# Performance work log

Hardware: AMD Instinct MI355X
Metric: run time of the kernel (lower is better)

Reference implementation:

```python
import jax, jax.numpy as jnp
import numpy as np

N_NODES = 50000
N_EDGES = 600000
DIM = 128


def setup_inputs() -> dict:
    key = jax.random.key(0)
    k1, k2, k3, k4, k5, k6 = jax.random.split(key, 6)
    return {
        "h_v": jax.random.normal(k1, (N_NODES, DIM), dtype=jnp.float32),
        "h_d": jax.random.normal(k2, (N_EDGES, DIM), dtype=jnp.float32),
        "W_pi": jax.random.normal(k3, (DIM, 1), dtype=jnp.float32) * (1.0 / np.sqrt(DIM)),
        "W_M": jax.random.normal(k4, (2 * DIM, 1), dtype=jnp.float32) * (1.0 / np.sqrt(2 * DIM)),
        "src": jax.random.randint(k5, (N_EDGES,), 0, N_NODES, dtype=jnp.int64) if jax.config.jax_enable_x64 else jax.random.randint(k5, (N_EDGES,), 0, N_NODES, dtype=jnp.int32),
        "dst": jax.random.randint(k6, (N_EDGES,), 0, N_NODES, dtype=jnp.int32),
    }


def reference(h_v, h_d, W_pi, W_M, src, dst):
    # Gather per-edge endpoint features: [E, dim]
    ft_s = h_v[src]
    ft_d = h_v[dst]
    prod = ft_s * ft_d                                   # u_mul_v
    # e = pi(src*dst*d): [E, 1]
    e = (prod * h_d) @ W_pi
    # mask = sigmoid(M(cat([src*dst, d]))): [E, 1]
    mask = jax.nn.sigmoid(jnp.concatenate([prod, h_d], axis=-1) @ W_M)
    logits = (e * mask)[:, 0]                            # [E]
    # edge_softmax grouped by destination node (DGL semantics)
    seg_max = jax.ops.segment_max(logits, dst, num_segments=N_NODES)
    ex = jnp.exp(logits - seg_max[dst])
    seg_sum = jax.ops.segment_sum(ex, dst, num_segments=N_NODES)
    a = ex / seg_sum[dst]                                # [E]
    # dropout_local is identity at inference
    # message m = ft_src * a; aggregate sum over incoming edges per dst node
    out = jax.ops.segment_sum(ft_s * a[:, None], dst, num_segments=N_NODES)
    return out
```

## Files before the change

### kernel.cpp

```cpp
#include <hip/hip_runtime.h>

#define NN 50000
#define NE 600000
#define DIM 128
#define NB 196


__global__ __launch_bounds__(256) void zero_counts_kernel(int* __restrict__ counts) {
    int i = blockIdx.x * 256 + threadIdx.x;
    if (i < NN) counts[i] = 0;
}

__global__ __launch_bounds__(256) void hist_kernel(const int* __restrict__ dst,
                                                   int* __restrict__ counts) {
    int e = blockIdx.x * 256 + threadIdx.x;
    if (e < NE) atomicAdd(&counts[dst[e]], 1);
}

__global__ __launch_bounds__(256) void scan_pass1_kernel(const int* __restrict__ counts,
                                                         int* __restrict__ offsets,
                                                         int* __restrict__ blockSums) {
    __shared__ int tmp[256];
    int tid = threadIdx.x;
    int i = blockIdx.x * 256 + tid;
    int v = (i < NN) ? counts[i] : 0;
    tmp[tid] = v;
    __syncthreads();
    #pragma unroll
    for (int off = 1; off < 256; off <<= 1) {
        int t = (tid >= off) ? tmp[tid - off] : 0;
        __syncthreads();
        tmp[tid] += t;
        __syncthreads();
    }
    int incl = tmp[tid];
    if (i < NN) offsets[i] = incl - v;
    if (tid == 255) blockSums[blockIdx.x] = incl;
}

__global__ __launch_bounds__(256) void scan_pass2_kernel(int* __restrict__ blockSums) {
    __shared__ int tmp[256];
    int tid = threadIdx.x;
    int v = (tid < NB) ? blockSums[tid] : 0;
    tmp[tid] = v;
    __syncthreads();
    #pragma unroll
    for (int off = 1; off < 256; off <<= 1) {
        int t = (tid >= off) ? tmp[tid - off] : 0;
        __syncthreads();
        tmp[tid] += t;
        __syncthreads();
    }
    if (tid < NB) blockSums[tid] = tmp[tid] - v;
}

__global__ __launch_bounds__(256) void scan_pass3_kernel(int* __restrict__ offsets,
                                                         const int* __restrict__ blockSums,
                                                         int* __restrict__ cursor) {
    int i = blockIdx.x * 256 + threadIdx.x;
    if (i < NN) {
        int o = offsets[i] + blockSums[i >> 8];
        offsets[i] = o;
        cursor[i] = o;
    }
    if (i == 0) offsets[NN] = NE;
}

__global__ __launch_bounds__(256) void scatter_kernel(const int* __restrict__ src,
                                                      const int* __restrict__ dst,
                                                      int* __restrict__ cursor,
                                                      int2* __restrict__ pairs) {
    int e = blockIdx.x * 256 + threadIdx.x;
    if (e >= NE) return;
    int d = dst[e];
    int pos = atomicAdd(&cursor[d], 1);
    pairs[pos] = make_int2(src[e], e);
}


__global__ __launch_bounds__(256) void node_fused_kernel(
    const float* __restrict__ h_v, const float* __restrict__ h_d,
    const float* __restrict__ W_pi, const float* __restrict__ W_M,
    const int* __restrict__ offsets, const int2* __restrict__ pairs,
    float* __restrict__ out) {
    int node = (blockIdx.x * 256 + threadIdx.x) >> 6;
    int lane = threadIdx.x & 63;
    if (node >= NN) return;
    int half = lane >> 5;
    int l32 = lane & 31;

    const float4 fd = ((const float4*)(h_v + (size_t)node * DIM))[l32];
    const float4 wp = ((const float4*)W_pi)[l32];
    const float4 m0 = ((const float4*)W_M)[l32];
    const float4 m1 = ((const float4*)(W_M + DIM))[l32];

    int beg = offsets[node];
    int end = offsets[node + 1];

    float4 acc = make_float4(0.0f, 0.0f, 0.0f, 0.0f);
    float ssum = 0.0f;
    for (int k = beg + half; k < end; k += 2) {
        int2 p = pairs[k];
        const float4 fs = ((const float4*)(h_v + (size_t)p.x * DIM))[l32];
        const float4 hd = ((const float4*)(h_d + (size_t)p.y * DIM))[l32];

        float px = fs.x * fd.x, py = fs.y * fd.y, pz = fs.z * fd.z, pw = fs.w * fd.w;
        float s1 = px * hd.x * wp.x + py * hd.y * wp.y + pz * hd.z * wp.z + pw * hd.w * wp.w;
        float s2 = px * m0.x + py * m0.y + pz * m0.z + pw * m0.w
                 + hd.x * m1.x + hd.y * m1.y + hd.z * m1.z + hd.w * m1.w;
        #pragma unroll
        for (int off = 16; off > 0; off >>= 1) {
            s1 += __shfl_xor(s1, off, 64);
            s2 += __shfl_xor(s2, off, 64);
        }
        float logit = s1 / (1.0f + __expf(-s2));
        float ex = __expf(logit);
        acc.x += fs.x * ex;
        acc.y += fs.y * ex;
        acc.z += fs.z * ex;
        acc.w += fs.w * ex;
        ssum += ex;
    }

    acc.x += __shfl_xor(acc.x, 32, 64);
    acc.y += __shfl_xor(acc.y, 32, 64);
    acc.z += __shfl_xor(acc.z, 32, 64);
    acc.w += __shfl_xor(acc.w, 32, 64);
    ssum  += __shfl_xor(ssum, 32, 64);

    if (half == 0) {
        float inv = (ssum > 0.0f) ? 1.0f / ssum : 0.0f;
        ((float4*)(out + (size_t)node * DIM))[l32] =
            make_float4(acc.x * inv, acc.y * inv, acc.z * inv, acc.w * inv);
    }
}


extern "C" void kernel_launch(void* const* d_in, const int* in_sizes, int n_in,
                              void* d_out, int out_size, void* d_ws, size_t ws_size,
                              hipStream_t stream) {
    const float* h_v  = (const float*)d_in[0];
    const float* h_d  = (const float*)d_in[1];
    const float* W_pi = (const float*)d_in[2];
    const float* W_M  = (const float*)d_in[3];
    const int*   src  = (const int*)d_in[4];
    const int*   dst  = (const int*)d_in[5];
    float* out = (float*)d_out;

    int* counts    = (int*)d_ws;
    int* offsets   = counts + NN;
    int* cursor    = offsets + NN + 1;
    int* blockSums = cursor + NN;
    int2* pairs    = (int2*)(((uintptr_t)(blockSums + 256) + 7) & ~(uintptr_t)7);

    zero_counts_kernel<<<NB, 256, 0, stream>>>(counts);
    hist_kernel<<<(NE + 255) / 256, 256, 0, stream>>>(dst, counts);
    scan_pass1_kernel<<<NB, 256, 0, stream>>>(counts, offsets, blockSums);
    scan_pass2_kernel<<<1, 256, 0, stream>>>(blockSums);
    scan_pass3_kernel<<<NB, 256, 0, stream>>>(offsets, blockSums, cursor);
    scatter_kernel<<<(NE + 255) / 256, 256, 0, stream>>>(src, dst, cursor, pairs);
    node_fused_kernel<<<(NN * 64 + 255) / 256, 256, 0, stream>>>(
        h_v, h_d, W_pi, W_M, offsets, pairs, out);
}
```

Measured before the change: 524.8 us.

## Software-pipeline edge row loads with wave-wide pair prefetch and nontemporal h_d

```diff
diff --git a/kernel.cpp b/kernel.cpp
--- a/kernel.cpp
+++ b/kernel.cpp
@@ -4,6 +4,8 @@
 #define NE 600000
 #define DIM 128
 #define NB 196
+
+typedef float v4f __attribute__((ext_vector_type(4)));
 
 
 __global__ __launch_bounds__(256) void zero_counts_kernel(int* __restrict__ counts) {
@@ -78,6 +80,13 @@
 }
 
 
+__device__ __forceinline__ v4f load_row(const float* p, int l32) {
+    return ((const v4f*)p)[l32];
+}
+__device__ __forceinline__ v4f load_row_nt(const float* p, int l32) {
+    return __builtin_nontemporal_load(((const v4f*)p) + l32);
+}
+
 __global__ __launch_bounds__(256) void node_fused_kernel(
     const float* __restrict__ h_v, const float* __restrict__ h_d,
     const float* __restrict__ W_pi, const float* __restrict__ W_M,
@@ -89,37 +98,66 @@
     int half = lane >> 5;
     int l32 = lane & 31;
 
-    const float4 fd = ((const float4*)(h_v + (size_t)node * DIM))[l32];
-    const float4 wp = ((const float4*)W_pi)[l32];
-    const float4 m0 = ((const float4*)W_M)[l32];
-    const float4 m1 = ((const float4*)(W_M + DIM))[l32];
+    const v4f fd = load_row(h_v + (size_t)node * DIM, l32);
+    const v4f wp = load_row(W_pi, l32);
+    const v4f m0 = load_row(W_M, l32);
+    const v4f m1 = load_row(W_M + DIM, l32);
 
     int beg = offsets[node];
-    int end = offsets[node + 1];
-
-    float4 acc = make_float4(0.0f, 0.0f, 0.0f, 0.0f);
+    int deg = offsets[node + 1] - beg;
+
+    v4f acc = {0.0f, 0.0f, 0.0f, 0.0f};
     float ssum = 0.0f;
-    for (int k = beg + half; k < end; k += 2) {
-        int2 p = pairs[k];
-        const float4 fs = ((const float4*)(h_v + (size_t)p.x * DIM))[l32];
-        const float4 hd = ((const float4*)(h_d + (size_t)p.y * DIM))[l32];
-
-        float px = fs.x * fd.x, py = fs.y * fd.y, pz = fs.z * fd.z, pw = fs.w * fd.w;
-        float s1 = px * hd.x * wp.x + py * hd.y * wp.y + pz * hd.z * wp.z + pw * hd.w * wp.w;
-        float s2 = px * m0.x + py * m0.y + pz * m0.z + pw * m0.w
-                 + hd.x * m1.x + hd.y * m1.y + hd.z * m1.z + hd.w * m1.w;
-        #pragma unroll
-        for (int off = 16; off > 0; off >>= 1) {
-            s1 += __shfl_xor(s1, off, 64);
-            s2 += __shfl_xor(s2, off, 64);
+
+    for (int base = 0; base < deg; base += 64) {
+        int tl = min(64, deg - base);
+        int kk = beg + base + ((lane < tl) ? lane : 0);
+        int2 myp = pairs[kk];
+
+        int j = half;
+        bool has0 = j < tl, has1 = (j + 2) < tl;
+        v4f fs0 = {}, hd0 = {}, fs1 = {}, hd1 = {};
+        if (has0) {
+            int s = __shfl(myp.x, j, 64), e = __shfl(myp.y, j, 64);
+            fs0 = load_row(h_v + (size_t)s * DIM, l32);
+            hd0 = load_row_nt(h_d + (size_t)e * DIM, l32);
         }
-        float logit = s1 / (1.0f + __expf(-s2));
-        float ex = __expf(logit);
-        acc.x += fs.x * ex;
-        acc.y += fs.y * ex;
-        acc.z += fs.z * ex;
-        acc.w += fs.w * ex;
-        ssum += ex;
+        if (has1) {
+            int s = __shfl(myp.x, j + 2, 64), e = __shfl(myp.y, j + 2, 64);
+            fs1 = load_row(h_v + (size_t)s * DIM, l32);
+            hd1 = load_row_nt(h_d + (size_t)e * DIM, l32);
+        }
+        while (has0) {
+            int jn = j + 4;
+            bool hasn = jn < tl;
+            v4f fsn = {}, hdn = {};
+            if (hasn) {
+                int s = __shfl(myp.x, jn, 64), e = __shfl(myp.y, jn, 64);
+                fsn = load_row(h_v + (size_t)s * DIM, l32);
+                hdn = load_row_nt(h_d + (size_t)e * DIM, l32);
+            }
+            float px = fs0.x * fd.x, py = fs0.y * fd.y,
+                  pz = fs0.z * fd.z, pw = fs0.w * fd.w;
+            float s1 = px * hd0.x * wp.x + py * hd0.y * wp.y
+                     + pz * hd0.z * wp.z + pw * hd0.w * wp.w;
+            float s2 = px * m0.x + py * m0.y + pz * m0.z + pw * m0.w
+                     + hd0.x * m1.x + hd0.y * m1.y + hd0.z * m1.z + hd0.w * m1.w;
+            #pragma unroll
+            for (int off = 16; off > 0; off >>= 1) {
+                s1 += __shfl_xor(s1, off, 64);
+                s2 += __shfl_xor(s2, off, 64);
+            }
+            float logit = s1 / (1.0f + __expf(-s2));
+            float ex = __expf(logit);
+            acc.x += fs0.x * ex;
+            acc.y += fs0.y * ex;
+            acc.z += fs0.z * ex;
+            acc.w += fs0.w * ex;
+            ssum += ex;
+            fs0 = fs1; hd0 = hd1; has0 = has1;
+            fs1 = fsn; hd1 = hdn; has1 = hasn;
+            j += 2;
+        }
     }
 
     acc.x += __shfl_xor(acc.x, 32, 64);
@@ -130,8 +168,8 @@
 
     if (half == 0) {
         float inv = (ssum > 0.0f) ? 1.0f / ssum : 0.0f;
-        ((float4*)(out + (size_t)node * DIM))[l32] =
-            make_float4(acc.x * inv, acc.y * inv, acc.z * inv, acc.w * inv);
+        v4f r = {acc.x * inv, acc.y * inv, acc.z * inv, acc.w * inv};
+        ((v4f*)(out + (size_t)node * DIM))[l32] = r;
     }
 }
 
```

Measured after the change: 529.3 us. Within noise of the previous version (+0.9%).
